# Kernel tuning notes

Hardware: AMD Instinct MI355X
Metric: run time of the kernel (lower is better)

Reference implementation:

```python
import jax, jax.numpy as jnp
import numpy as np

EPS = 1e-4  # constant referenced as EPS in the original source (Performer stabilizer)
B, N, D = 4, 4096, 1024
H, M = 16, 256
DH = D // H  # 64


def _gaussian_orthogonal_random_matrix(n_rows, n_cols, rng):
    # blocks of QR-orthogonal matrices, rows scaled by norms of gaussian rows
    blocks = []
    for _ in range(n_rows // n_cols):
        q, _ = np.linalg.qr(rng.standard_normal((n_cols, n_cols)))
        blocks.append(q.T)
    rem = n_rows - (n_rows // n_cols) * n_cols
    if rem > 0:
        q, _ = np.linalg.qr(rng.standard_normal((n_cols, n_cols)))
        blocks.append(q.T[:rem])
    final = np.concatenate(blocks, axis=0)
    mult = np.linalg.norm(rng.standard_normal((n_rows, n_cols)), axis=1)
    return (mult[:, None] * final).astype(np.float32)


def setup_inputs() -> dict:
    key = jax.random.key(0)
    kq, kk, kv, kw = jax.random.split(key, 4)
    q = jax.random.normal(kq, (B, N, D), jnp.float32)
    k = jax.random.normal(kk, (B, N, D), jnp.float32)
    v = jax.random.normal(kv, (B, N, D), jnp.float32)
    W = jax.random.normal(kw, (D, D), jnp.float32) * 0.02  # to_out weight [out, in]
    b = jnp.zeros((D,), jnp.float32)
    proj = jnp.asarray(_gaussian_orthogonal_random_matrix(M, DH, np.random.default_rng(0)))
    return {"q": q, "k": k, "v": v, "W": W, "b": b, "proj": proj}


def _softmax_kernel(data, proj, is_query):
    # data: [B,H,N,Dh], proj: [M,Dh]
    dh = data.shape[-1]
    data_scale = dh ** (-0.25)
    scale = proj.shape[0] ** (-0.5)
    dp = jnp.einsum('bhnd,md->bhnm', data * data_scale, proj)  # [B,H,N,M]
    dn = (jnp.sum(data * data, axis=-1) * (0.5 * data_scale ** 2))[..., None]
    axes = (-1, -2) if is_query else (-1,)
    m = jax.lax.stop_gradient(jnp.max(dp, axis=axes, keepdims=True))
    return scale * jnp.exp(dp - dn - m + EPS)


def reference(q, k, v, W, b, proj):
    # split heads: b n (h d) -> b h n d
    def split(t):
        return t.reshape(B, N, H, DH).transpose(0, 2, 1, 3)
    qh, kh, vh = split(q), split(k), split(v)
    qp = _softmax_kernel(qh, proj, True)    # [B,H,N,M]
    kp = _softmax_kernel(kh, proj, False)   # [B,H,N,M]
    context = jnp.einsum('bhnm,bhne->bhme', kp, vh)          # [B,H,M,Dh]
    d_inv = 1.0 / jnp.einsum('bhnm,bhm->bhn', qp, kp.sum(axis=-2))
    out = jnp.einsum('bhme,bhnm,bhn->bhne', context, qp, d_inv)  # [B,H,N,Dh]
    out = out.transpose(0, 2, 1, 3).reshape(B, N, D)  # b h n d -> b n (h d)
    out = out @ W.T + b  # nn.Linear; dropout is identity at eval / p=0
    return out
```

## Files before the change

kernel.cpp:

```cpp
#include <hip/hip_runtime.h>
#include <hip/hip_bf16.h>
#include <stdint.h>

#define DATA_SCALE 0.35355339059327373f
#define DN_SCALE   0.0625f

typedef __bf16 bf16x8 __attribute__((ext_vector_type(8)));
typedef float  f32x4  __attribute__((ext_vector_type(4)));

static __device__ __forceinline__ unsigned short f2bf(float f) {
    union { __bf16 b; unsigned short u; } t;
    t.b = (__bf16)f;
    return t.u;
}

static __device__ __forceinline__ f32x4 mfma16(bf16x8 a, bf16x8 b, f32x4 c) {
    return __builtin_amdgcn_mfma_f32_16x16x32_bf16(a, b, c, 0, 0, 0);
}

static __device__ __forceinline__ void gload16(const void* g, void* lds) {
    __builtin_amdgcn_global_load_lds(
        (const __attribute__((address_space(1))) unsigned int*)g,
        (__attribute__((address_space(3))) unsigned int*)lds, 16, 0, 0);
}

union U8 { unsigned short s[8]; __bf16 b[8]; unsigned int u[4]; bf16x8 v; };
union P4 { __bf16 b[4]; uint2 u2; };

__global__ __launch_bounds__(256) void k_prep(const float* __restrict__ W,
                                              const float* __restrict__ proj,
                                              unsigned short* __restrict__ Wb,
                                              unsigned short* __restrict__ projs,
                                              unsigned short* __restrict__ projs_swz) {
    int i = blockIdx.x * 256 + threadIdx.x;
    if (i < 1024 * 1024) Wb[i] = f2bf(W[i]);
    if (i < 256 * 64) {
        const int row = i >> 6, col = i & 63;
        unsigned short v = f2bf(proj[i] * DATA_SCALE);
        projs[i] = v;
        projs_swz[row * 64 + (col ^ ((row & 7) << 3))] = v;
    }
}

__global__ __launch_bounds__(256) void k_ctx(const float* __restrict__ kg,
                                             const float* __restrict__ vg,
                                             const unsigned short* __restrict__ projs,
                                             const unsigned short* __restrict__ projz,
                                             float* __restrict__ ctx_part,
                                             float* __restrict__ ksum_part,
                                             int cshift, int ntiles) {
    const int bh = blockIdx.x >> cshift, chunk = blockIdx.x & ((1 << cshift) - 1);
    const int b = bh >> 4, h = bh & 15;
    const int tid = threadIdx.x;
    const int w = tid >> 6, lane = tid & 63, l15 = lane & 15, hh = lane >> 4;

    __shared__ __align__(16) unsigned short kpT[256][72];
    __shared__ __align__(16) unsigned short VT[64][72];
    __shared__ __align__(16) unsigned short pjL[256 * 64];

#pragma unroll
    for (int i = 0; i < 8; ++i) {
        const int blk = i*4 + w;
        gload16((const char*)projz + blk*1024 + lane*16, (char*)pjL + blk*1024);
    }

    bf16x8 pb0r[16];
#pragma unroll
    for (int ni = 0; ni < 16; ++ni)
        pb0r[ni] = *(const bf16x8*)(projs + (size_t)(16*ni + l15) * 64 + 8*hh);

    f32x4 cacc[4][4];
#pragma unroll
    for (int i = 0; i < 4; ++i)
#pragma unroll
        for (int j = 0; j < 4; ++j) cacc[i][j] = (f32x4){0.f, 0.f, 0.f, 0.f};
    float ksacc[16];
#pragma unroll
    for (int i = 0; i < 16; ++i) ksacc[i] = 0.f;

    const size_t rowoff = (size_t)(b * 4096 + chunk * ntiles * 64) * 1024 + h * 64;

    const float* vbase = vg + rowoff + (size_t)lane * 1024 + w * 16;
    const float* kbase = kg + rowoff + (size_t)(16*w + l15) * 1024 + hh * 8;

    float4 v0 = *(const float4*)(vbase);
    float4 v1 = *(const float4*)(vbase + 4);
    float4 v2 = *(const float4*)(vbase + 8);
    float4 v3 = *(const float4*)(vbase + 12);
    float4 k0 = *(const float4*)(kbase);
    float4 k1 = *(const float4*)(kbase + 4);
    float4 k2 = *(const float4*)(kbase + 32);
    float4 k3 = *(const float4*)(kbase + 36);

    for (int tt = 0; tt < ntiles; ++tt) {
        __syncthreads();

        {
            const int n = lane, cs = w * 16;
            VT[cs+ 0][n] = f2bf(v0.x); VT[cs+ 1][n] = f2bf(v0.y);
            VT[cs+ 2][n] = f2bf(v0.z); VT[cs+ 3][n] = f2bf(v0.w);
            VT[cs+ 4][n] = f2bf(v1.x); VT[cs+ 5][n] = f2bf(v1.y);
            VT[cs+ 6][n] = f2bf(v1.z); VT[cs+ 7][n] = f2bf(v1.w);
            VT[cs+ 8][n] = f2bf(v2.x); VT[cs+ 9][n] = f2bf(v2.y);
            VT[cs+10][n] = f2bf(v2.z); VT[cs+11][n] = f2bf(v2.w);
            VT[cs+12][n] = f2bf(v3.x); VT[cs+13][n] = f2bf(v3.y);
            VT[cs+14][n] = f2bf(v3.z); VT[cs+15][n] = f2bf(v3.w);
        }

        float s2 = k0.x*k0.x + k0.y*k0.y + k0.z*k0.z + k0.w*k0.w
                 + k1.x*k1.x + k1.y*k1.y + k1.z*k1.z + k1.w*k1.w
                 + k2.x*k2.x + k2.y*k2.y + k2.z*k2.z + k2.w*k2.w
                 + k3.x*k3.x + k3.y*k3.y + k3.z*k3.z + k3.w*k3.w;
        s2 += __shfl_xor(s2, 16);
        s2 += __shfl_xor(s2, 32);
        U8 a0, a1;
        a0.b[0]=(__bf16)k0.x; a0.b[1]=(__bf16)k0.y; a0.b[2]=(__bf16)k0.z; a0.b[3]=(__bf16)k0.w;
        a0.b[4]=(__bf16)k1.x; a0.b[5]=(__bf16)k1.y; a0.b[6]=(__bf16)k1.z; a0.b[7]=(__bf16)k1.w;
        a1.b[0]=(__bf16)k2.x; a1.b[1]=(__bf16)k2.y; a1.b[2]=(__bf16)k2.z; a1.b[3]=(__bf16)k2.w;
        a1.b[4]=(__bf16)k3.x; a1.b[5]=(__bf16)k3.y; a1.b[6]=(__bf16)k3.z; a1.b[7]=(__bf16)k3.w;

        if (tt + 1 < ntiles) {
            const float* vs = vbase + (size_t)(tt + 1) * 65536;
            v0 = *(const float4*)(vs);
            v1 = *(const float4*)(vs + 4);
            v2 = *(const float4*)(vs + 8);
            v3 = *(const float4*)(vs + 12);
            const float* ks_ = kbase + (size_t)(tt + 1) * 65536;
            k0 = *(const float4*)(ks_);
            k1 = *(const float4*)(ks_ + 4);
            k2 = *(const float4*)(ks_ + 32);
            k3 = *(const float4*)(ks_ + 36);
        }

        f32x4 sacc[16];
#pragma unroll
        for (int i = 0; i < 16; ++i) sacc[i] = (f32x4){0.f, 0.f, 0.f, 0.f};
#pragma unroll
        for (int ni = 0; ni < 16; ++ni)
            sacc[ni] = mfma16(a0.v, pb0r[ni], sacc[ni]);
#pragma unroll
        for (int ni = 0; ni < 16; ++ni) {
            bf16x8 pb1 = *(const bf16x8*)&pjL[(16*ni + l15)*64 + ((32 + 8*hh) ^ ((l15 & 7) << 3))];
            sacc[ni] = mfma16(a1.v, pb1, sacc[ni]);
        }

        float pm[4];
#pragma unroll
        for (int r = 0; r < 4; ++r) {
            float m01 = fmaxf(sacc[0][r], sacc[1][r]);
#pragma unroll
            for (int ni = 2; ni < 16; ++ni) m01 = fmaxf(m01, sacc[ni][r]);
            pm[r] = m01;
        }
#pragma unroll
        for (int msk = 1; msk <= 8; msk <<= 1)
#pragma unroll
            for (int r = 0; r < 4; ++r)
                pm[r] = fmaxf(pm[r], __shfl_xor(pm[r], msk));
        float offv[4];
#pragma unroll
        for (int r = 0; r < 4; ++r) {
            float s2r = __shfl(s2, (lane & 48) + 4*hh + r);
            offv[r] = pm[r] + DN_SCALE * s2r;
        }

#pragma unroll
        for (int ni = 0; ni < 16; ++ni) {
            float e0 = __expf(sacc[ni][0] - offv[0]);
            float e1 = __expf(sacc[ni][1] - offv[1]);
            float e2 = __expf(sacc[ni][2] - offv[2]);
            float e3 = __expf(sacc[ni][3] - offv[3]);
            ksacc[ni] += e0 + e1 + e2 + e3;
            P4 pk;
            pk.b[0]=(__bf16)e0; pk.b[1]=(__bf16)e1; pk.b[2]=(__bf16)e2; pk.b[3]=(__bf16)e3;
            const int colp = (16*w + 4*hh) ^ (8*(ni & 7));
            *(uint2*)&kpT[16*ni + l15][colp] = pk.u2;
        }
        __syncthreads();

#pragma unroll
        for (int ks = 0; ks < 2; ++ks) {
            bf16x8 am[4], bv[4];
#pragma unroll
            for (int mi = 0; mi < 4; ++mi) {
                const int row = 64*w + 16*mi + l15;
                const int s = (4*w + mi) & 7;
                am[mi] = *(const bf16x8*)&kpT[row][8*((4*ks + hh) ^ s)];
            }
#pragma unroll
            for (int ni = 0; ni < 4; ++ni)
                bv[ni] = *(const bf16x8*)&VT[16*ni + l15][ks*32 + 8*hh];
#pragma unroll
            for (int mi = 0; mi < 4; ++mi)
#pragma unroll
                for (int ni = 0; ni < 4; ++ni)
                    cacc[mi][ni] = mfma16(am[mi], bv[ni], cacc[mi][ni]);
        }
    }

#pragma unroll
    for (int ni = 0; ni < 16; ++ni) {
        ksacc[ni] += __shfl_xor(ksacc[ni], 16);
        ksacc[ni] += __shfl_xor(ksacc[ni], 32);
    }
    __syncthreads();
    float* ksW = (float*)&VT[0][0];
    if (hh == 0) {
#pragma unroll
        for (int ni = 0; ni < 16; ++ni)
            ksW[w*256 + 16*ni + l15] = ksacc[ni];
    }
    __syncthreads();
    const int pc = blockIdx.x;
    if (tid < 256)
        ksum_part[(size_t)pc * 256 + tid] = ksW[tid] + ksW[256 + tid]
                                          + ksW[512 + tid] + ksW[768 + tid];
    float* cp = ctx_part + (size_t)pc * 256 * 64;
#pragma unroll
    for (int mi = 0; mi < 4; ++mi)
#pragma unroll
        for (int ni = 0; ni < 4; ++ni)
#pragma unroll
            for (int r = 0; r < 4; ++r)
                cp[(64*w + 16*mi + 4*hh + r) * 64 + 16*ni + l15] = cacc[mi][ni][r];
}

__global__ __launch_bounds__(256) void k_reduce(const float* __restrict__ ctx_part,
                                                const float* __restrict__ ksum_part,
                                                unsigned short* __restrict__ ctxT,
                                                float* __restrict__ ksum, int nchunk) {
    const int bh = blockIdx.x >> 3, part = blockIdx.x & 7;
    const int t = threadIdx.x;
    const int m = part*32 + (t & 31);
    const int dq = t >> 5;
    const int mb = m >> 4;
    const int c = 32*(mb >> 1) + 8*((m >> 2) & 3) + 4*(mb & 1) + (m & 3);
    const float* cp = ctx_part + (size_t)bh * nchunk * 16384 + m*64 + dq*8;
    f32x4 s[2];
#pragma unroll
    for (int j = 0; j < 2; ++j) s[j] = *(const f32x4*)(cp + j*4);
    for (int cch = 1; cch < nchunk; ++cch) {
        const float* cc = cp + (size_t)cch * 16384;
#pragma unroll
        for (int j = 0; j < 2; ++j) {
            f32x4 a = *(const f32x4*)(cc + j*4);
            s[j] += a;
        }
    }
    unsigned short* ct = ctxT + (size_t)bh * 16384;
#pragma unroll
    for (int j = 0; j < 2; ++j)
#pragma unroll
        for (int e = 0; e < 4; ++e) {
            const int dh = dq*8 + j*4 + e;
            ct[dh * 256 + (c ^ ((dh & 7) << 3))] = f2bf(s[j][e]);
        }
    if (t < 32) {
        const int m2 = part*32 + t;
        const float* kp_ = ksum_part + (size_t)bh * nchunk * 256;
        float ks = 0.f;
        for (int cch = 0; cch < nchunk; ++cch) ks += kp_[cch*256 + m2];
        ksum[(size_t)bh * 256 + m2] = ks;
    }
}

__global__ __launch_bounds__(256) void k_qout(const float* __restrict__ qg,
                                              const unsigned short* __restrict__ projs_swz,
                                              const unsigned short* __restrict__ ctxT,
                                              const float* __restrict__ ksum,
                                              unsigned short* __restrict__ attn) {
    const int lb = (blockIdx.x & 7) * 128 + (blockIdx.x >> 3);
    const int bh = lb >> 4, rg = lb & 15;
    const int b = bh >> 4, h = bh & 15;
    const int tid = threadIdx.x;
    const int w = tid >> 6, lane = tid & 63, l15 = lane & 15, hh = lane >> 4;

    __shared__ __align__(16) unsigned short pjL[256 * 64];
    __shared__ __align__(16) unsigned short ctxL[64 * 256];

#pragma unroll
    for (int i = 0; i < 8; ++i) {
        const int blk = i*4 + w;
        gload16((const char*)projs_swz + blk*1024 + lane*16, (char*)pjL + blk*1024);
        gload16((const char*)(ctxT + (size_t)bh * 16384) + blk*1024 + lane*16,
                (char*)ctxL + blk*1024);
    }

    f32x4 ksr4[16];
#pragma unroll
    for (int mb = 0; mb < 16; ++mb)
        ksr4[mb] = *(const f32x4*)(ksum + (size_t)bh * 256 + 16*mb + 4*hh);

    const float* qtile = qg + (size_t)(b*4096 + rg*256 + 16*w + l15) * 1024 + h*64 + hh*8;

    float4 qA[4], qB[4];
    qA[0] = *(const float4*)(qtile);
    qA[1] = *(const float4*)(qtile + 4);
    qA[2] = *(const float4*)(qtile + 32);
    qA[3] = *(const float4*)(qtile + 36);

    __syncthreads();

#pragma unroll
    for (int t = 0; t < 4; ++t) {
        const float4* qc = (t & 1) ? qB : qA;
        float4*       qn = (t & 1) ? qA : qB;

        U8 a0, a1;
        a0.b[0]=(__bf16)qc[0].x; a0.b[1]=(__bf16)qc[0].y; a0.b[2]=(__bf16)qc[0].z; a0.b[3]=(__bf16)qc[0].w;
        a0.b[4]=(__bf16)qc[1].x; a0.b[5]=(__bf16)qc[1].y; a0.b[6]=(__bf16)qc[1].z; a0.b[7]=(__bf16)qc[1].w;
        a1.b[0]=(__bf16)qc[2].x; a1.b[1]=(__bf16)qc[2].y; a1.b[2]=(__bf16)qc[2].z; a1.b[3]=(__bf16)qc[2].w;
        a1.b[4]=(__bf16)qc[3].x; a1.b[5]=(__bf16)qc[3].y; a1.b[6]=(__bf16)qc[3].z; a1.b[7]=(__bf16)qc[3].w;

        if (t < 3) {
            const float* qs = qtile + (size_t)(t + 1) * 65536;
            qn[0] = *(const float4*)(qs);
            qn[1] = *(const float4*)(qs + 4);
            qn[2] = *(const float4*)(qs + 32);
            qn[3] = *(const float4*)(qs + 36);
        }

        f32x4 sacc[16];
#pragma unroll
        for (int i = 0; i < 16; ++i) sacc[i] = (f32x4){0.f, 0.f, 0.f, 0.f};
#pragma unroll
        for (int mb = 0; mb < 16; ++mb) {
            bf16x8 pb0 = *(const bf16x8*)&pjL[(16*mb + l15)*64 + ((8*hh) ^ ((l15 & 7) << 3))];
            sacc[mb] = mfma16(pb0, a0.v, sacc[mb]);
        }
#pragma unroll
        for (int mb = 0; mb < 16; ++mb) {
            bf16x8 pb1 = *(const bf16x8*)&pjL[(16*mb + l15)*64 + ((32 + 8*hh) ^ ((l15 & 7) << 3))];
            sacc[mb] = mfma16(pb1, a1.v, sacc[mb]);
        }

        float dp = 0.f;
        uint2 p[16];
#pragma unroll
        for (int mb = 0; mb < 16; ++mb) {
            float e0 = __expf(sacc[mb][0]);
            float e1 = __expf(sacc[mb][1]);
            float e2 = __expf(sacc[mb][2]);
            float e3 = __expf(sacc[mb][3]);
            dp += e0*ksr4[mb][0] + e1*ksr4[mb][1] + e2*ksr4[mb][2] + e3*ksr4[mb][3];
            P4 pk;
            pk.b[0]=(__bf16)e0; pk.b[1]=(__bf16)e1; pk.b[2]=(__bf16)e2; pk.b[3]=(__bf16)e3;
            p[mb] = pk.u2;
        }

        f32x4 nacc[4];
#pragma unroll
        for (int i = 0; i < 4; ++i) nacc[i] = (f32x4){0.f, 0.f, 0.f, 0.f};
#pragma unroll
        for (int ks = 0; ks < 8; ++ks) {
            U8 bf;
            bf.u[0] = p[2*ks].x;  bf.u[1] = p[2*ks].y;
            bf.u[2] = p[2*ks+1].x; bf.u[3] = p[2*ks+1].y;
#pragma unroll
            for (int mi = 0; mi < 4; ++mi) {
                bf16x8 av = *(const bf16x8*)&ctxL[(16*mi + l15)*256
                                                  + ((ks*32 + 8*hh) ^ ((l15 & 7) << 3))];
                nacc[mi] = mfma16(av, bf.v, nacc[mi]);
            }
        }

        dp += __shfl_xor(dp, 16);
        dp += __shfl_xor(dp, 32);
        const float rd = 1.f / dp;

        const int grow = rg*256 + t*64 + 16*w + l15;
        unsigned short* dst = attn + (size_t)(b*4096 + grow) * 1024 + h*64 + 4*hh;
#pragma unroll
        for (int mi = 0; mi < 4; ++mi) {
            P4 o;
            o.b[0] = (__bf16)(nacc[mi][0] * rd);
            o.b[1] = (__bf16)(nacc[mi][1] * rd);
            o.b[2] = (__bf16)(nacc[mi][2] * rd);
            o.b[3] = (__bf16)(nacc[mi][3] * rd);
            *(uint2*)(dst + 16*mi) = o.u2;
        }
    }
}

__global__ __launch_bounds__(256) void k_linear(const unsigned short* __restrict__ A,
                                                const unsigned short* __restrict__ Wb,
                                                const float* __restrict__ bias,
                                                float* __restrict__ out) {
    const int lb = (blockIdx.x & 7) * 128 + (blockIdx.x >> 3);
    const int bm = lb >> 3, bn = lb & 7;
    const int tid = threadIdx.x;
    const int w = tid >> 6, lane = tid & 63, l15 = lane & 15, hh = lane >> 4;
    const int wm = w >> 1, wn = w & 1;
    const int m0 = bm * 128, n0 = bn * 128;

    __shared__ __align__(16) unsigned short As[128 * 64];
    __shared__ __align__(16) unsigned short Bs[128 * 64];

    const int srow = lane >> 3;
    const int scol = (lane & 7) * 8;

    f32x4 acc[4][4];
#pragma unroll
    for (int i = 0; i < 4; ++i)
#pragma unroll
        for (int j = 0; j < 4; ++j) acc[i][j] = (f32x4){0.f, 0.f, 0.f, 0.f};

    for (int kt = 0; kt < 16; ++kt) {
        __syncthreads();
#pragma unroll
        for (int i = 0; i < 4; ++i) {
            const int rr = (w*4 + i)*8 + srow;
            gload16(A  + (size_t)(m0 + rr) * 1024 + kt*64 + scol, &As[(w*4 + i) * 512]);
            gload16(Wb + (size_t)(n0 + rr) * 1024 + kt*64 + scol, &Bs[(w*4 + i) * 512]);
        }
        __syncthreads();
#pragma unroll
        for (int ks = 0; ks < 2; ++ks) {
            bf16x8 af[4], bw[4];
#pragma unroll
            for (int mi = 0; mi < 4; ++mi)
                af[mi] = *(const bf16x8*)&As[(wm*64 + 16*mi + l15) * 64 + ks*32 + 8*hh];
#pragma unroll
            for (int ni = 0; ni < 4; ++ni)
                bw[ni] = *(const bf16x8*)&Bs[(wn*64 + 16*ni + l15) * 64 + ks*32 + 8*hh];
#pragma unroll
            for (int mi = 0; mi < 4; ++mi)
#pragma unroll
                for (int ni = 0; ni < 4; ++ni)
                    acc[mi][ni] = mfma16(af[mi], bw[ni], acc[mi][ni]);
        }
    }

    float bs[4];
#pragma unroll
    for (int ni = 0; ni < 4; ++ni) bs[ni] = bias[n0 + wn*64 + 16*ni + l15];
#pragma unroll
    for (int mi = 0; mi < 4; ++mi) {
        const int row = m0 + wm*64 + 16*mi + 4*hh;
#pragma unroll
        for (int r = 0; r < 4; ++r) {
            float* o = out + (size_t)(row + r) * 1024 + n0 + wn*64;
#pragma unroll
            for (int ni = 0; ni < 4; ++ni)
                o[16*ni + l15] = acc[mi][ni][r] + bs[ni];
        }
    }
}

extern "C" void kernel_launch(void* const* d_in, const int* in_sizes, int n_in,
                              void* d_out, int out_size, void* d_ws, size_t ws_size,
                              hipStream_t stream) {
    const float* q    = (const float*)d_in[0];
    const float* k    = (const float*)d_in[1];
    const float* v    = (const float*)d_in[2];
    const float* W    = (const float*)d_in[3];
    const float* bias = (const float*)d_in[4];
    const float* proj = (const float*)d_in[5];
    float* out = (float*)d_out;

    int nchunk = 8;
    while (nchunk > 4) {
        size_t need = 33554432ull + 2097152 + 2097152 + 65536 + 32768 + 32768
                    + (size_t)nchunk * 65536
                    + (size_t)nchunk * 4194304
                    + 4096;
        if (need <= ws_size) break;
        nchunk >>= 1;
    }
    const int cshift = (nchunk == 8) ? 3 : 2;
    const int ntiles = 64 / nchunk;

    char* ws = (char*)d_ws;
    size_t off = 0;
    unsigned short* attn  = (unsigned short*)(ws + off); off += 33554432;
    unsigned short* ctxT  = (unsigned short*)(ws + off); off += 2097152;
    unsigned short* Wb    = (unsigned short*)(ws + off); off += 2097152;
    float*          ksum  = (float*)(ws + off);          off += 65536;
    unsigned short* projs = (unsigned short*)(ws + off); off += 32768;
    unsigned short* projz = (unsigned short*)(ws + off); off += 32768;
    float*          ksump = (float*)(ws + off);          off += (size_t)nchunk * 65536;
    float*          ctxp  = (float*)(ws + off);          off += (size_t)nchunk * 4194304;

    k_prep<<<dim3(4096), dim3(256), 0, stream>>>(W, proj, Wb, projs, projz);
    k_ctx<<<dim3(64 * nchunk), dim3(256), 0, stream>>>(k, v, projs, projz, ctxp, ksump,
                                                       cshift, ntiles);
    k_reduce<<<dim3(512), dim3(256), 0, stream>>>(ctxp, ksump, ctxT, ksum, nchunk);
    k_qout<<<dim3(1024), dim3(256), 0, stream>>>(q, projz, ctxT, ksum, attn);
    k_linear<<<dim3(1024), dim3(256), 0, stream>>>(attn, Wb, bias, out);
}
```

Before: 172.7 us.

## Fuse chunk reduction into k_ctx via last-block atomic counter

```diff
diff --git a/kernel.cpp b/kernel.cpp
--- a/kernel.cpp
+++ b/kernel.cpp
@@ -48,6 +48,9 @@
                                              const unsigned short* __restrict__ projz,
                                              float* __restrict__ ctx_part,
                                              float* __restrict__ ksum_part,
+                                             unsigned short* __restrict__ ctxT,
+                                             float* __restrict__ ksum,
+                                             int* __restrict__ ctr,
                                              int cshift, int ntiles) {
     const int bh = blockIdx.x >> cshift, chunk = blockIdx.x & ((1 << cshift) - 1);
     const int b = bh >> 4, h = bh & 15;
@@ -57,6 +60,7 @@
     __shared__ __align__(16) unsigned short kpT[256][72];
     __shared__ __align__(16) unsigned short VT[64][72];
     __shared__ __align__(16) unsigned short pjL[256 * 64];
+    __shared__ int lastFlag;
 
 #pragma unroll
     for (int i = 0; i < 8; ++i) {
@@ -223,44 +227,52 @@
 #pragma unroll
             for (int r = 0; r < 4; ++r)
                 cp[(64*w + 16*mi + 4*hh + r) * 64 + 16*ni + l15] = cacc[mi][ni][r];
-}
-
-__global__ __launch_bounds__(256) void k_reduce(const float* __restrict__ ctx_part,
-                                                const float* __restrict__ ksum_part,
-                                                unsigned short* __restrict__ ctxT,
-                                                float* __restrict__ ksum, int nchunk) {
-    const int bh = blockIdx.x >> 3, part = blockIdx.x & 7;
-    const int t = threadIdx.x;
-    const int m = part*32 + (t & 31);
-    const int dq = t >> 5;
-    const int mb = m >> 4;
-    const int c = 32*(mb >> 1) + 8*((m >> 2) & 3) + 4*(mb & 1) + (m & 3);
-    const float* cp = ctx_part + (size_t)bh * nchunk * 16384 + m*64 + dq*8;
-    f32x4 s[2];
-#pragma unroll
-    for (int j = 0; j < 2; ++j) s[j] = *(const f32x4*)(cp + j*4);
-    for (int cch = 1; cch < nchunk; ++cch) {
-        const float* cc = cp + (size_t)cch * 16384;
-#pragma unroll
-        for (int j = 0; j < 2; ++j) {
-            f32x4 a = *(const f32x4*)(cc + j*4);
-            s[j] += a;
-        }
-    }
+
+    const int nchunk = 1 << cshift;
+    __threadfence();
+    __syncthreads();
+    if (tid == 0) {
+        int old = atomicAdd(&ctr[bh], 1);
+        lastFlag = (old == nchunk - 1);
+    }
+    __syncthreads();
+    if (!lastFlag) return;
+    __threadfence();
+
+    const float* basep = ctx_part + (size_t)bh * nchunk * 16384;
     unsigned short* ct = ctxT + (size_t)bh * 16384;
-#pragma unroll
-    for (int j = 0; j < 2; ++j)
-#pragma unroll
-        for (int e = 0; e < 4; ++e) {
-            const int dh = dq*8 + j*4 + e;
-            ct[dh * 256 + (c ^ ((dh & 7) << 3))] = f2bf(s[j][e]);
-        }
-    if (t < 32) {
-        const int m2 = part*32 + t;
-        const float* kp_ = ksum_part + (size_t)bh * nchunk * 256;
-        float ks = 0.f;
-        for (int cch = 0; cch < nchunk; ++cch) ks += kp_[cch*256 + m2];
-        ksum[(size_t)bh * 256 + m2] = ks;
+    const float* kpp = ksum_part + (size_t)bh * nchunk * 256;
+#pragma unroll 1
+    for (int part = 0; part < 8; ++part) {
+        const int m = part*32 + (tid & 31);
+        const int dq = tid >> 5;
+        const int mb = m >> 4;
+        const int c = 32*(mb >> 1) + 8*((m >> 2) & 3) + 4*(mb & 1) + (m & 3);
+        const float* cp2 = basep + m*64 + dq*8;
+        f32x4 s[2];
+#pragma unroll
+        for (int j = 0; j < 2; ++j) s[j] = *(const f32x4*)(cp2 + j*4);
+        for (int cch = 1; cch < nchunk; ++cch) {
+            const float* cc = cp2 + (size_t)cch * 16384;
+#pragma unroll
+            for (int j = 0; j < 2; ++j) {
+                f32x4 a = *(const f32x4*)(cc + j*4);
+                s[j] += a;
+            }
+        }
+#pragma unroll
+        for (int j = 0; j < 2; ++j)
+#pragma unroll
+            for (int e = 0; e < 4; ++e) {
+                const int dh = dq*8 + j*4 + e;
+                ct[dh * 256 + (c ^ ((dh & 7) << 3))] = f2bf(s[j][e]);
+            }
+        if (tid < 32) {
+            const int m2 = part*32 + tid;
+            float ks = 0.f;
+            for (int cch = 0; cch < nchunk; ++cch) ks += kpp[cch*256 + m2];
+            ksum[(size_t)bh * 256 + m2] = ks;
+        }
     }
 }
 
@@ -460,7 +472,7 @@
 
     int nchunk = 8;
     while (nchunk > 4) {
-        size_t need = 33554432ull + 2097152 + 2097152 + 65536 + 32768 + 32768
+        size_t need = 33554432ull + 2097152 + 2097152 + 65536 + 32768 + 32768 + 4096
                     + (size_t)nchunk * 65536
                     + (size_t)nchunk * 4194304
                     + 4096;
@@ -478,13 +490,14 @@
     float*          ksum  = (float*)(ws + off);          off += 65536;
     unsigned short* projs = (unsigned short*)(ws + off); off += 32768;
     unsigned short* projz = (unsigned short*)(ws + off); off += 32768;
+    int*            ctr   = (int*)(ws + off);            off += 4096;
     float*          ksump = (float*)(ws + off);          off += (size_t)nchunk * 65536;
     float*          ctxp  = (float*)(ws + off);          off += (size_t)nchunk * 4194304;
 
+    hipMemsetAsync(ctr, 0, 64 * sizeof(int), stream);
     k_prep<<<dim3(4096), dim3(256), 0, stream>>>(W, proj, Wb, projs, projz);
     k_ctx<<<dim3(64 * nchunk), dim3(256), 0, stream>>>(k, v, projs, projz, ctxp, ksump,
-                                                       cshift, ntiles);
-    k_reduce<<<dim3(512), dim3(256), 0, stream>>>(ctxp, ksump, ctxT, ksum, nchunk);
+                                                       ctxT, ksum, ctr, cshift, ntiles);
     k_qout<<<dim3(1024), dim3(256), 0, stream>>>(q, projz, ctxT, ksum, attn);
     k_linear<<<dim3(1024), dim3(256), 0, stream>>>(attn, Wb, bias, out);
 }
```

Result: slower. 359.7 us (+108.3%).
